# Optimization experiments

Measured on AMD Instinct MI355X. Metric: run time of the kernel, lower is better.

The kernel has to match this reference:

```python
import jax, jax.numpy as jnp
import numpy as np

B, S, D, H = 2, 2048, 1024, 16
DK = D // H

def setup_inputs() -> dict:
    key = jax.random.key(0)
    k1, k2, k3 = jax.random.split(key, 3)
    std = 2.0 / (D + 3 * D)
    x = jax.random.normal(k1, (B, S, D), dtype=jnp.float32)
    W_qkv = jax.random.normal(k2, (3 * D, D), dtype=jnp.float32) * std
    W_out = jax.random.normal(k3, (D, D), dtype=jnp.float32) * (2.0 / (2 * D))
    return {"x": x, "W_qkv": W_qkv, "W_out": W_out}

def reference(x, W_qkv, W_out):
    # fused QKV projection: [..., d_in] x [d_out, d_in] -> [..., d_out]
    proj = jnp.einsum('bsd,ed->bse', x, W_qkv)               # [B,S,3*H*DK]
    proj = proj.reshape(B, S, 3, H, DK)
    q = proj[:, :, 0].transpose(0, 2, 1, 3)                  # [B,H,S,DK]
    k = proj[:, :, 1].transpose(0, 2, 1, 3)
    v = proj[:, :, 2].transpose(0, 2, 1, 3)
    scores = jnp.einsum('bhnd,bhmd->bhnm', q, k) / jnp.sqrt(jnp.float32(DK))
    causal = jnp.tril(jnp.ones((S, S), dtype=bool))
    scores = jnp.where(causal, scores, -jnp.inf)
    attn = jax.nn.softmax(scores, axis=-1)
    out = jnp.einsum('bhnm,bhmd->bhnd', attn, v)             # [B,H,S,DK]
    out = out.transpose(0, 2, 1, 3).reshape(B, S, H * DK)
    return jnp.einsum('bsd,ed->bse', out, W_out)             # [B,S,D]
```

## Files before the change

kernel.cpp:

```cpp
#include <hip/hip_runtime.h>
#include <hip/hip_bf16.h>
#include <stdint.h>

typedef __attribute__((ext_vector_type(8))) __bf16 bf16x8;
typedef __attribute__((ext_vector_type(8))) short  short8;
typedef __attribute__((ext_vector_type(4))) float  f32x4;

#define MFMA16(a, b, c) __builtin_amdgcn_mfma_f32_16x16x32_bf16((a), (b), (c), 0, 0, 0)

__device__ __forceinline__ unsigned short f32_bf16(float f) {
  union { float f; unsigned u; } v; v.f = f;
  unsigned r = v.u + 0x7FFFu + ((v.u >> 16) & 1u);
  return (unsigned short)(r >> 16);
}

__device__ __forceinline__ void gload16(const unsigned short* g, unsigned short* l) {
  __builtin_amdgcn_global_load_lds(
      (const __attribute__((address_space(1))) unsigned int*)(g),
      (__attribute__((address_space(3))) unsigned int*)(l), 16, 0, 0);
}

__global__ void cvt3_kernel(const float* __restrict__ a, int na4,
                            const float* __restrict__ b, int nb4,
                            const float* __restrict__ c, int nc4,
                            unsigned short* __restrict__ oa,
                            unsigned short* __restrict__ ob,
                            unsigned short* __restrict__ oc) {
  int total = na4 + nb4 + nc4;
  for (int i = blockIdx.x * blockDim.x + threadIdx.x; i < total; i += gridDim.x * blockDim.x) {
    const float* src; unsigned short* dst; int j = i;
    if (j < na4) { src = a; dst = oa; }
    else if (j - na4 < nb4) { j -= na4; src = b; dst = ob; }
    else { j -= na4 + nb4; src = c; dst = oc; }
    float4 v = reinterpret_cast<const float4*>(src)[j];
    ushort4 o4;
    o4.x = f32_bf16(v.x); o4.y = f32_bf16(v.y);
    o4.z = f32_bf16(v.z); o4.w = f32_bf16(v.w);
    reinterpret_cast<ushort4*>(dst)[j] = o4;
  }
}

__global__ __launch_bounds__(512, 2) void gemm_qkv_8ph(const unsigned short* __restrict__ A,
                                                       const unsigned short* __restrict__ Bm,
                                                       unsigned short* __restrict__ qkv) {
  extern __shared__ unsigned short SM[];
  const int tid  = threadIdx.x;
  const int lane = tid & 63;
  const int w    = tid >> 6;
  const int wr   = w >> 2, wc = w & 3;
  const int l16  = lane & 15, lh = lane >> 4;
  const int sw   = l16 & 7;
  const int m0   = blockIdx.y * 256;
  const int n0   = blockIdx.x * 256;

  f32x4 acc[8][4];
#pragma unroll
  for (int mi = 0; mi < 8; ++mi)
#pragma unroll
    for (int ni = 0; ni < 4; ++ni) acc[mi][ni] = 0.f;

  const int r0 = tid >> 3,         h0 = (tid & 7) ^ (r0 & 7);
  const int r1 = (tid + 512) >> 3, h1 = (tid & 7) ^ (r1 & 7);
  const unsigned short* Asrc[2][2];
  const unsigned short* Bsrc[2][2];
  Asrc[0][0] = A + (size_t)(m0 + r0) * 1024 + h0 * 8;
  Asrc[0][1] = A + (size_t)(m0 + r1) * 1024 + h1 * 8;
  Asrc[1][0] = A + (size_t)(m0 + 128 + r0) * 1024 + h0 * 8;
  Asrc[1][1] = A + (size_t)(m0 + 128 + r1) * 1024 + h1 * 8;
  Bsrc[0][0] = Bm + (size_t)(n0 + r0) * 1024 + h0 * 8;
  Bsrc[0][1] = Bm + (size_t)(n0 + r1) * 1024 + h1 * 8;
  Bsrc[1][0] = Bm + (size_t)(n0 + 128 + r0) * 1024 + h0 * 8;
  Bsrc[1][1] = Bm + (size_t)(n0 + 128 + r1) * 1024 + h1 * 8;
  const int ld0 = (w * 64) * 8;
  const int ld1 = (512 + w * 64) * 8;

#define STAGE_A(buf, h, U) do { \
    gload16(Asrc[h][0] + (U) * 64, SM + (buf) * 32768 + (h) * 8192 + ld0); \
    gload16(Asrc[h][1] + (U) * 64, SM + (buf) * 32768 + (h) * 8192 + ld1); } while (0)
#define STAGE_B(buf, h, U) do { \
    gload16(Bsrc[h][0] + (U) * 64, SM + (buf) * 32768 + 16384 + (h) * 8192 + ld0); \
    gload16(Bsrc[h][1] + (U) * 64, SM + (buf) * 32768 + 16384 + (h) * 8192 + ld1); } while (0)

  STAGE_A(0, 0, 0); STAGE_A(0, 1, 0);
  STAGE_B(0, 0, 0); STAGE_B(0, 1, 0);
  STAGE_B(1, 0, 1); STAGE_B(1, 1, 1);
  asm volatile("s_waitcnt vmcnt(4)" ::: "memory");
  __builtin_amdgcn_s_barrier();

  const int NT = 16;
#pragma unroll 2
  for (int U = 0; U < NT; ++U) {
    const int b = U & 1;
    const unsigned short* Ab = SM + b * 32768 + wr * 8192;
    const unsigned short* Bb = SM + b * 32768 + 16384 + (wc >> 1) * 8192;
    const int rB = (wc & 1) * 64;
    bf16x8 bfr[4][2], af[2][2];

#define LDA(i, j) (*(const bf16x8*)(Ab + (((i) * 16 + l16) * 8 + (((j) * 4 + lh) ^ sw)) * 8))
#define LDB(n, j) (*(const bf16x8*)(Bb + (((rB + (n) * 16 + l16)) * 8 + (((j) * 4 + lh) ^ sw)) * 8))
#define PHASE_MFMA(p) \
    __builtin_amdgcn_s_setprio(1); \
    _Pragma("unroll") \
    for (int n = 0; n < 4; ++n) { \
      acc[2*(p)][n]   = MFMA16(af[0][0], bfr[n][0], acc[2*(p)][n]); \
      acc[2*(p)][n]   = MFMA16(af[0][1], bfr[n][1], acc[2*(p)][n]); \
      acc[2*(p)+1][n] = MFMA16(af[1][0], bfr[n][0], acc[2*(p)+1][n]); \
      acc[2*(p)+1][n] = MFMA16(af[1][1], bfr[n][1], acc[2*(p)+1][n]); \
    } \
    __builtin_amdgcn_s_setprio(0);

    af[0][0] = LDA(0, 0); af[0][1] = LDA(0, 1);
    af[1][0] = LDA(1, 0); af[1][1] = LDA(1, 1);
#pragma unroll
    for (int n = 0; n < 4; ++n) { bfr[n][0] = LDB(n, 0); bfr[n][1] = LDB(n, 1); }
    if (U + 1 < NT) STAGE_A(b ^ 1, 0, U + 1);
    __builtin_amdgcn_s_barrier();
    PHASE_MFMA(0)
    __builtin_amdgcn_s_barrier();
    af[0][0] = LDA(2, 0); af[0][1] = LDA(2, 1);
    af[1][0] = LDA(3, 0); af[1][1] = LDA(3, 1);
    if (U + 1 < NT) STAGE_A(b ^ 1, 1, U + 1);
    __builtin_amdgcn_s_barrier();
    PHASE_MFMA(1)
    __builtin_amdgcn_s_barrier();
    af[0][0] = LDA(4, 0); af[0][1] = LDA(4, 1);
    af[1][0] = LDA(5, 0); af[1][1] = LDA(5, 1);
    if (U + 2 < NT) STAGE_B(b, 0, U + 2);
    __builtin_amdgcn_s_barrier();
    PHASE_MFMA(2)
    __builtin_amdgcn_s_barrier();
    af[0][0] = LDA(6, 0); af[0][1] = LDA(6, 1);
    af[1][0] = LDA(7, 0); af[1][1] = LDA(7, 1);
    if (U + 2 < NT) STAGE_B(b, 1, U + 2);
    __builtin_amdgcn_s_barrier();
    PHASE_MFMA(3)
    asm volatile("s_waitcnt vmcnt(4)" ::: "memory");
    __builtin_amdgcn_s_barrier();
#undef LDA
#undef LDB
#undef PHASE_MFMA
  }

  __syncthreads();
  unsigned short* Ep = SM + w * 8192;
  const int gn0 = n0 + wc * 64;
  const int cc  = gn0 >> 10;
  const int hh2 = (gn0 & 1023) >> 6;
  const int gm0 = m0 + wr * 128;
  const int bb2 = gm0 >> 11;
  const int ss0 = gm0 & 2047;
  const int bh2 = bb2 * 16 + hh2;

  if (cc < 2) {
    const float qsc = (cc == 0) ? 0.18033688f : 1.0f;
#pragma unroll
    for (int mi = 0; mi < 8; ++mi)
#pragma unroll
      for (int ni = 0; ni < 4; ++ni)
#pragma unroll
        for (int r = 0; r < 4; ++r) {
          int row = mi * 16 + lh * 4 + r;
          int col = (ni * 16 + l16) ^ (lh << 3);
          Ep[row * 64 + col] = f32_bf16(acc[mi][ni][r] * qsc);
        }
    unsigned short* qk = qkv + (((size_t)cc * 32 + bh2) * 2048 + ss0) * 64;
#pragma unroll
    for (int it = 0; it < 16; ++it) {
      int ci = it * 64 + lane;
      int row = ci >> 3, c = ci & 7;
      short8 vv = *(const short8*)(Ep + row * 64 + ((c ^ ((row >> 2) & 3)) * 8));
      *(short8*)(qk + (size_t)row * 64 + c * 8) = vv;
    }
  } else {
#pragma unroll
    for (int mi = 0; mi < 8; ++mi)
#pragma unroll
      for (int ni = 0; ni < 4; ++ni) {
        int dk = ni * 16 + l16;
        int ssl = mi * 16 + lh * 4;
        unsigned lo, hi;
        asm("v_cvt_pk_bf16_f32 %0, %1, %2" : "=v"(lo) : "v"(acc[mi][ni][0]), "v"(acc[mi][ni][1]));
        asm("v_cvt_pk_bf16_f32 %0, %1, %2" : "=v"(hi) : "v"(acc[mi][ni][2]), "v"(acc[mi][ni][3]));
        int off = dk * 128 + (ssl ^ ((dk & 7) << 3));
        *(uint2*)(Ep + off) = make_uint2(lo, hi);
      }
    unsigned short* vt = qkv + (size_t)8388608 + (size_t)bh2 * 64 * 2048 + ss0;
#pragma unroll
    for (int it = 0; it < 16; ++it) {
      int ci = it * 64 + lane;
      int dk = ci >> 4, c = ci & 15;
      short8 vv = *(const short8*)(Ep + dk * 128 + ((c ^ (dk & 7)) * 8));
      *(short8*)(vt + (size_t)dk * 2048 + c * 8) = vv;
    }
  }
#undef STAGE_A
#undef STAGE_B
}

__global__ __launch_bounds__(256) void gemm_out(const unsigned short* __restrict__ A,
                                                const unsigned short* __restrict__ Bm,
                                                float* __restrict__ C,
                                                int M, int N, int K) {
  extern __shared__ unsigned short SM[];
  unsigned short* As = SM;
  unsigned short* Bs = SM + 4096;
  const int tid  = threadIdx.x;
  const int lane = tid & 63;
  const int wid  = tid >> 6;
  const int wr   = wid >> 1, wc = wid & 1;
  const int l16  = lane & 15, lh = lane >> 4;
  const int m0   = blockIdx.y * 128;
  const int n0   = blockIdx.x * 128;

  f32x4 acc[4][4];
#pragma unroll
  for (int mi = 0; mi < 4; ++mi)
#pragma unroll
    for (int ni = 0; ni < 4; ++ni) acc[mi][ni] = 0.f;

  const int c0 = tid, c1 = 256 + tid;
  const unsigned short* a0 = A + (size_t)(m0 + (c0 >> 2)) * K + (c0 & 3) * 8;
  const unsigned short* a1 = A + (size_t)(m0 + (c1 >> 2)) * K + (c1 & 3) * 8;
  const unsigned short* b0 = Bm + (size_t)(n0 + (c0 >> 2)) * K + (c0 & 3) * 8;
  const unsigned short* b1 = Bm + (size_t)(n0 + (c1 >> 2)) * K + (c1 & 3) * 8;
  const int d0 = wid * 64 * 8;
  const int d1 = (256 + wid * 64) * 8;

  for (int k0 = 0; k0 < K; k0 += 32) {
    __syncthreads();
    gload16(a0 + k0, As + d0);
    gload16(a1 + k0, As + d1);
    gload16(b0 + k0, Bs + d0);
    gload16(b1 + k0, Bs + d1);
    __syncthreads();
    bf16x8 af[4], bfr[4];
#pragma unroll
    for (int i = 0; i < 4; ++i) {
      af[i]  = *(const bf16x8*)(As + (wr * 64 + i * 16 + l16) * 32 + lh * 8);
      bfr[i] = *(const bf16x8*)(Bs + (wc * 64 + i * 16 + l16) * 32 + lh * 8);
    }
#pragma unroll
    for (int mi = 0; mi < 4; ++mi)
#pragma unroll
      for (int ni = 0; ni < 4; ++ni)
        acc[mi][ni] = MFMA16(af[mi], bfr[ni], acc[mi][ni]);
  }

  __syncthreads();
  float* Ef = (float*)(SM + wid * 4096);
  const int gm0 = m0 + wr * 64;
  const int gn0 = n0 + wc * 64;
#pragma unroll
  for (int p = 0; p < 2; ++p) {
#pragma unroll
    for (int mi = 0; mi < 4; ++mi)
#pragma unroll
      for (int q = 0; q < 2; ++q) {
        int ni = 2 * p + q;
#pragma unroll
        for (int r = 0; r < 4; ++r) {
          int row = mi * 16 + lh * 4 + r;
          int col = (q * 16 + l16) ^ ((row & 7) << 2);
          Ef[row * 32 + col] = acc[mi][ni][r];
        }
      }
#pragma unroll
    for (int it = 0; it < 8; ++it) {
      int ci = it * 64 + lane;
      int row = ci >> 3, c4 = ci & 7;
      float4 vv = *(const float4*)(Ef + row * 32 + ((c4 * 4) ^ ((row & 7) << 2)));
      *(float4*)(&C[(size_t)(gm0 + row) * N + gn0 + p * 32 + c4 * 4]) = vv;
    }
  }
}

__device__ const signed char JQT[48] = {31,31,30,15, 30,29,29,28,14, 28,27,27,26,13, 26,25,25,24,12,
                                        24,23,23,22,11, 22,21,21,20,10, 20,19,19,18, 9, 18,17,17,16, 8,
                                        16, 7, 6, 5, 4, 3, 2, 1, 0};
__device__ const signed char JS0[48] = { 0,16, 0, 0, 16, 0,15, 0, 0, 15, 0,14, 0, 0, 14, 0,13, 0, 0,
                                        13, 0,12, 0, 0, 12, 0,11, 0, 0, 11, 0,10, 0, 0, 10, 0, 9, 0, 0,
                                         9, 0, 0, 0, 0, 0, 0, 0, 0};
__device__ const signed char JNT[48] = {16,16,16,16, 15,15,15,15,15, 14,14,14,14,14, 13,13,13,13,13,
                                        12,12,12,12,12, 11,11,11,11,11, 10,10,10,10,10,  9, 9, 9, 9, 9,
                                         8, 8, 7, 6, 5, 4, 3, 2, 1};
__device__ const signed char JSL[48] = {30,31,28,-1, 29,26,27,24,-1, 25,22,23,20,-1, 21,18,19,16,-1,
                                        17,14,15,12,-1, 13,10,11, 8,-1,  9, 6, 7, 4,-1,  5, 2, 3, 0,-1,
                                         1,-1,-1,-1,-1,-1,-1,-1,-1};

__global__ __launch_bounds__(256) void attn_kernel(const unsigned short* __restrict__ Qg,
                                                   const unsigned short* __restrict__ Kg,
                                                   const unsigned short* __restrict__ Vtg,
                                                   unsigned short* __restrict__ Og,
                                                   char* __restrict__ parts) {
  __shared__ unsigned short Ks[2][64 * 64];
  __shared__ unsigned short Vs[2][64 * 64];
  __shared__ unsigned short Pl[4][16 * 64];

  const int tid  = threadIdx.x;
  const int lane = tid & 63;
  const int w    = tid >> 6;
  const int l16  = lane & 15, lh = lane >> 4;
  const int sw   = l16 & 7;

  const int jb   = blockIdx.x >> 5;
  const int bh   = blockIdx.x & 31;
  const int qt   = JQT[jb];
  const int ts0  = JS0[jb];
  const int tend = ts0 + JNT[jb];
  const int slot = JSL[jb];
  const int bb   = bh >> 4, hh = bh & 15;
  const int qb   = qt * 64;
  const int wqb  = qb + w * 16;

  const unsigned short* Qh = Qg + (size_t)bh * (2048 * 64);
  const unsigned short* Kh = Kg + (size_t)bh * (2048 * 64);
  const unsigned short* Vh = Vtg + (size_t)bh * (64 * 2048);

  bf16x8 qf[2];
#pragma unroll
  for (int h2 = 0; h2 < 2; ++h2)
    qf[h2] = *(const bf16x8*)(Qh + (size_t)(wqb + l16) * 64 + h2 * 32 + lh * 8);

  float mreg = 0.f;
  float ll   = 0.f;
  f32x4 o[4];
#pragma unroll
  for (int f = 0; f < 4; ++f) o[f] = 0.f;

  const int sA = tid, sB = tid + 256;
  const int rA = sA >> 3, hA = (sA & 7) ^ (rA & 7);
  const int rB = sB >> 3, hB = (sB & 7) ^ (rB & 7);
  const unsigned short* kSrcA = Kh + rA * 64 + hA * 8;
  const unsigned short* kSrcB = Kh + rB * 64 + hB * 8;
  const unsigned short* vSrcA = Vh + (size_t)rA * 2048 + hA * 8;
  const unsigned short* vSrcB = Vh + (size_t)rB * 2048 + hB * 8;
  const int ldsA = w * 64 * 8;
  const int ldsB = (256 + w * 64) * 8;

  gload16(kSrcA + (size_t)(ts0 * 64) * 64, &Ks[0][ldsA]);
  gload16(kSrcB + (size_t)(ts0 * 64) * 64, &Ks[0][ldsB]);
  gload16(vSrcA + ts0 * 64, &Vs[0][ldsA]);
  gload16(vSrcB + ts0 * 64, &Vs[0][ldsB]);
  __syncthreads();

  for (int t = ts0; t < tend; ++t) {
    const int kv0 = t * 64;
    const int cur = (t - ts0) & 1;
    if (t + 1 < tend) {
      const int nk = kv0 + 64;
      gload16(kSrcA + (size_t)nk * 64, &Ks[cur ^ 1][ldsA]);
      gload16(kSrcB + (size_t)nk * 64, &Ks[cur ^ 1][ldsB]);
      gload16(vSrcA + nk, &Vs[cur ^ 1][ldsA]);
      gload16(vSrcB + nk, &Vs[cur ^ 1][ldsB]);
    }

    {
      const unsigned short* Kb = Ks[cur];
      const unsigned short* Vb = Vs[cur];

      f32x4 st[4];
#pragma unroll
      for (int tt = 0; tt < 4; ++tt) {
        const unsigned short* krow = Kb + (tt * 16 + l16) * 64;
        bf16x8 kf0 = *(const bf16x8*)(krow + ((lh ^ sw) * 8));
        bf16x8 kf1 = *(const bf16x8*)(krow + (((lh + 4) ^ sw) * 8));
        f32x4 a = {0.f, 0.f, 0.f, 0.f};
        a = MFMA16(kf0, qf[0], a);
        a = MFMA16(kf1, qf[1], a);
        st[tt] = a;
      }

      if (kv0 + 63 > wqb) {
        int qrow = wqb + l16;
#pragma unroll
        for (int tt = 0; tt < 4; ++tt) {
          int kvb = kv0 + tt * 16 + lh * 4;
#pragma unroll
          for (int r = 0; r < 4; ++r)
            if (kvb + r > qrow) st[tt][r] = -__builtin_inff();
        }
      }

      float pm = fmaxf(fmaxf(st[0][0], st[0][1]), fmaxf(st[0][2], st[0][3]));
#pragma unroll
      for (int tt = 1; tt < 4; ++tt)
        pm = fmaxf(pm, fmaxf(fmaxf(st[tt][0], st[tt][1]), fmaxf(st[tt][2], st[tt][3])));
      if (!__all(pm <= mreg + 8.f)) {
        float t0 = pm;
        t0 = fmaxf(t0, __shfl_xor(t0, 16));
        t0 = fmaxf(t0, __shfl_xor(t0, 32));
        float mn = fmaxf(mreg, t0);
        float er = exp2f(mreg - mn);
        mreg = mn;
        ll *= er;
#pragma unroll
        for (int r = 0; r < 4; ++r) {
          float e = __shfl(er, lh * 4 + r);
#pragma unroll
          for (int f = 0; f < 4; ++f) o[f][r] *= e;
        }
      }

      unsigned short* Pw = Pl[w];
      int rbase = l16 * 64;
      float ps = 0.f;
#pragma unroll
      for (int tt = 0; tt < 4; ++tt) {
        float p0 = exp2f(st[tt][0] - mreg);
        float p1 = exp2f(st[tt][1] - mreg);
        float p2 = exp2f(st[tt][2] - mreg);
        float p3 = exp2f(st[tt][3] - mreg);
        ps += (p0 + p1) + (p2 + p3);
        unsigned lo, hi;
        asm("v_cvt_pk_bf16_f32 %0, %1, %2" : "=v"(lo) : "v"(p0), "v"(p1));
        asm("v_cvt_pk_bf16_f32 %0, %1, %2" : "=v"(hi) : "v"(p2), "v"(p3));
        int c8 = tt * 2 + (lh >> 1);
        int off = rbase + ((c8 ^ sw) << 3) + (lh & 1) * 4;
        *(uint2*)(Pw + off) = make_uint2(lo, hi);
      }
      float rs = ps;
      rs += __shfl_xor(rs, 16);
      rs += __shfl_xor(rs, 32);
      ll += rs;

      bf16x8 pf0 = *(const bf16x8*)(Pw + rbase + ((lh ^ sw) * 8));
      bf16x8 pf1 = *(const bf16x8*)(Pw + rbase + (((lh + 4) ^ sw) * 8));
#pragma unroll
      for (int f = 0; f < 4; ++f) {
        const unsigned short* vrow = Vb + (f * 16 + l16) * 64;
        bf16x8 vf0 = *(const bf16x8*)(vrow + ((lh ^ sw) * 8));
        bf16x8 vf1 = *(const bf16x8*)(vrow + (((lh + 4) ^ sw) * 8));
        o[f] = MFMA16(pf0, vf0, o[f]);
        o[f] = MFMA16(pf1, vf1, o[f]);
      }
    }
    __syncthreads();
  }

  if (slot < 0) {
    unsigned short* op = Og + (size_t)bb * 2048 * 1024 + (size_t)hh * 64;
#pragma unroll
    for (int r = 0; r < 4; ++r) {
      float linv = 1.f / __shfl(ll, lh * 4 + r);
      int row = wqb + lh * 4 + r;
#pragma unroll
      for (int f = 0; f < 4; ++f)
        op[(size_t)row * 1024 + f * 16 + l16] = f32_bf16(o[f][r] * linv);
    }
  } else {
    char* pb = parts + (size_t)(bh * 32 + slot) * 8704;
    float* pl = (float*)pb;
    float* pmv = pl + 64;
    unsigned short* pO = (unsigned short*)(pb + 512);
    float lv[4], mv[4];
#pragma unroll
    for (int r = 0; r < 4; ++r) {
      lv[r] = __shfl(ll, lh * 4 + r);
      mv[r] = __shfl(mreg, lh * 4 + r);
    }
    if (l16 == 0) {
#pragma unroll
      for (int r = 0; r < 4; ++r) {
        pl[w * 16 + lh * 4 + r]  = lv[r];
        pmv[w * 16 + lh * 4 + r] = mv[r];
      }
    }
#pragma unroll
    for (int r = 0; r < 4; ++r)
#pragma unroll
      for (int f = 0; f < 4; ++f)
        pO[(w * 16 + lh * 4 + r) * 64 + f * 16 + l16] = f32_bf16(o[f][r]);
  }
}

__global__ __launch_bounds__(256) void merge_kernel(const char* __restrict__ parts,
                                                    unsigned short* __restrict__ Og) {
  const int task = blockIdx.x;
  const int bh = task & 31, qi = task >> 5;
  const int qt = 16 + qi;
  const int bb = bh >> 4, hh = bh & 15;
  const int tid = threadIdx.x;
  const int r = tid >> 2, q = tid & 3;

  const char* pb1 = parts + (size_t)(bh * 32 + 2 * qi) * 8704;
  const char* pb2 = parts + (size_t)(bh * 32 + 2 * qi + 1) * 8704;
  const float* l1p = (const float*)pb1;
  const float* l2p = (const float*)pb2;
  float lv1 = l1p[r], mv1 = l1p[64 + r];
  float lv2 = l2p[r], mv2 = l2p[64 + r];
  float mx = fmaxf(mv1, mv2);
  float w1 = exp2f(mv1 - mx), w2 = exp2f(mv2 - mx);
  float inv = 1.f / (lv1 * w1 + lv2 * w2);
  float s1 = w1 * inv, s2 = w2 * inv;

  const unsigned short* O1 = (const unsigned short*)(pb1 + 512) + r * 64 + q * 16;
  const unsigned short* O2 = (const unsigned short*)(pb2 + 512) + r * 64 + q * 16;
  short8 a0 = *(const short8*)(O1);
  short8 a1 = *(const short8*)(O1 + 8);
  short8 b0 = *(const short8*)(O2);
  short8 b1 = *(const short8*)(O2 + 8);

  unsigned outw[8];
#pragma unroll
  for (int i = 0; i < 4; ++i) {
    float x0 = __builtin_bit_cast(float, ((unsigned)(unsigned short)a0[2 * i]) << 16) * s1 +
               __builtin_bit_cast(float, ((unsigned)(unsigned short)b0[2 * i]) << 16) * s2;
    float x1 = __builtin_bit_cast(float, ((unsigned)(unsigned short)a0[2 * i + 1]) << 16) * s1 +
               __builtin_bit_cast(float, ((unsigned)(unsigned short)b0[2 * i + 1]) << 16) * s2;
    asm("v_cvt_pk_bf16_f32 %0, %1, %2" : "=v"(outw[i]) : "v"(x0), "v"(x1));
    float y0 = __builtin_bit_cast(float, ((unsigned)(unsigned short)a1[2 * i]) << 16) * s1 +
               __builtin_bit_cast(float, ((unsigned)(unsigned short)b1[2 * i]) << 16) * s2;
    float y1 = __builtin_bit_cast(float, ((unsigned)(unsigned short)a1[2 * i + 1]) << 16) * s1 +
               __builtin_bit_cast(float, ((unsigned)(unsigned short)b1[2 * i + 1]) << 16) * s2;
    asm("v_cvt_pk_bf16_f32 %0, %1, %2" : "=v"(outw[4 + i]) : "v"(y0), "v"(y1));
  }
  unsigned short* op = Og + ((size_t)bb * 2048 + qt * 64 + r) * 1024 + hh * 64 + q * 16;
  *(uint4*)(op)     = make_uint4(outw[0], outw[1], outw[2], outw[3]);
  *(uint4*)(op + 8) = make_uint4(outw[4], outw[5], outw[6], outw[7]);
}

extern "C" void kernel_launch(void* const* d_in, const int* in_sizes, int n_in,
                              void* d_out, int out_size, void* d_ws, size_t ws_size,
                              hipStream_t stream) {
  const float* x    = (const float*)d_in[0];
  const float* Wqkv = (const float*)d_in[1];
  const float* Wout = (const float*)d_in[2];
  float* out = (float*)d_out;

  char* ws = (char*)d_ws;
  unsigned short* xb  = (unsigned short*)(ws);
  unsigned short* wqb = (unsigned short*)(ws + (size_t)8 * 1024 * 1024);
  unsigned short* wob = (unsigned short*)(ws + (size_t)14 * 1024 * 1024);
  unsigned short* qkv = (unsigned short*)(ws + (size_t)16 * 1024 * 1024);
  unsigned short* att = (unsigned short*)(ws + (size_t)40 * 1024 * 1024);
  char* parts = ws;

  static bool attr_set = false;
  if (!attr_set) {
    hipFuncSetAttribute((const void*)gemm_qkv_8ph,
                        hipFuncAttributeMaxDynamicSharedMemorySize, 131072);
    attr_set = true;
  }

  cvt3_kernel<<<2048, 256, 0, stream>>>(x, 4194304 / 4, Wqkv, 3145728 / 4,
                                        Wout, 1048576 / 4, xb, wqb, wob);

  gemm_qkv_8ph<<<dim3(12, 16), 512, 131072, stream>>>(xb, wqb, qkv);

  const unsigned short* Qp  = qkv;
  const unsigned short* Kp  = qkv + 4194304;
  const unsigned short* Vtp = qkv + 8388608;
  attn_kernel<<<1536, 256, 0, stream>>>(Qp, Kp, Vtp, att, parts);
  merge_kernel<<<512, 256, 0, stream>>>(parts, att);

  gemm_out<<<dim3(8, 32), 256, 32768, stream>>>(att, wob, out, 4096, 1024, 1024);
}
```

Before: 118.3 us.

## Rewrite attention inner loop with 32x32 MFMA and split-KV warps

After: 118.1 us. About the same (-0.1%).

```diff
diff --git a/kernel.cpp b/kernel.cpp
--- a/kernel.cpp
+++ b/kernel.cpp
@@ -2,11 +2,13 @@
 #include <hip/hip_bf16.h>
 #include <stdint.h>
 
-typedef __attribute__((ext_vector_type(8))) __bf16 bf16x8;
-typedef __attribute__((ext_vector_type(8))) short  short8;
-typedef __attribute__((ext_vector_type(4))) float  f32x4;
+typedef __attribute__((ext_vector_type(8)))  __bf16 bf16x8;
+typedef __attribute__((ext_vector_type(8)))  short  short8;
+typedef __attribute__((ext_vector_type(4)))  float  f32x4;
+typedef __attribute__((ext_vector_type(16))) float  f32x16;
 
 #define MFMA16(a, b, c) __builtin_amdgcn_mfma_f32_16x16x32_bf16((a), (b), (c), 0, 0, 0)
+#define MFMA32(a, b, c) __builtin_amdgcn_mfma_f32_32x32x16_bf16((a), (b), (c), 0, 0, 0)
 
 __device__ __forceinline__ unsigned short f32_bf16(float f) {
   union { float f; unsigned u; } v; v.f = f;
@@ -294,13 +296,13 @@
                                                    char* __restrict__ parts) {
   __shared__ unsigned short Ks[2][64 * 64];
   __shared__ unsigned short Vs[2][64 * 64];
-  __shared__ unsigned short Pl[4][16 * 64];
 
   const int tid  = threadIdx.x;
   const int lane = tid & 63;
   const int w    = tid >> 6;
-  const int l16  = lane & 15, lh = lane >> 4;
-  const int sw   = l16 & 7;
+  const int wq   = w & 1, wkv = w >> 1;
+  const int l31  = lane & 31, hi = lane >> 5;
+  const int rx0  = (l31 ^ (l31 >> 3)) & 7;
 
   const int jb   = blockIdx.x >> 5;
   const int bh   = blockIdx.x & 31;
@@ -310,31 +312,28 @@
   const int slot = JSL[jb];
   const int bb   = bh >> 4, hh = bh & 15;
   const int qb   = qt * 64;
-  const int wqb  = qb + w * 16;
+  const int qcol = qb + wq * 32 + l31;
 
   const unsigned short* Qh = Qg + (size_t)bh * (2048 * 64);
   const unsigned short* Kh = Kg + (size_t)bh * (2048 * 64);
   const unsigned short* Vh = Vtg + (size_t)bh * (64 * 2048);
 
-  bf16x8 qf[2];
-#pragma unroll
-  for (int h2 = 0; h2 < 2; ++h2)
-    qf[h2] = *(const bf16x8*)(Qh + (size_t)(wqb + l16) * 64 + h2 * 32 + lh * 8);
-
-  float mreg = 0.f;
-  float ll   = 0.f;
-  f32x4 o[4];
-#pragma unroll
-  for (int f = 0; f < 4; ++f) o[f] = 0.f;
+  bf16x8 qf[4];
+#pragma unroll
+  for (int ks = 0; ks < 4; ++ks)
+    qf[ks] = *(const bf16x8*)(Qh + (size_t)qcol * 64 + ks * 16 + hi * 8);
+
+  f32x16 o0 = 0.f, o1 = 0.f;
+  float mreg = 0.f, ll = 0.f;
 
   const int sA = tid, sB = tid + 256;
-  const int rA = sA >> 3, hA = (sA & 7) ^ (rA & 7);
-  const int rB = sB >> 3, hB = (sB & 7) ^ (rB & 7);
+  const int rA = sA >> 3, hA = (sA & 7) ^ ((rA ^ (rA >> 3)) & 7);
+  const int rB = sB >> 3, hB = (sB & 7) ^ ((rB ^ (rB >> 3)) & 7);
   const unsigned short* kSrcA = Kh + rA * 64 + hA * 8;
   const unsigned short* kSrcB = Kh + rB * 64 + hB * 8;
   const unsigned short* vSrcA = Vh + (size_t)rA * 2048 + hA * 8;
   const unsigned short* vSrcB = Vh + (size_t)rB * 2048 + hB * 8;
-  const int ldsA = w * 64 * 8;
+  const int ldsA = (w * 64) * 8;
   const int ldsB = (256 + w * 64) * 8;
 
   gload16(kSrcA + (size_t)(ts0 * 64) * 64, &Ks[0][ldsA]);
@@ -353,123 +352,135 @@
       gload16(vSrcA + nk, &Vs[cur ^ 1][ldsA]);
       gload16(vSrcB + nk, &Vs[cur ^ 1][ldsB]);
     }
-
-    {
-      const unsigned short* Kb = Ks[cur];
-      const unsigned short* Vb = Vs[cur];
-
-      f32x4 st[4];
-#pragma unroll
-      for (int tt = 0; tt < 4; ++tt) {
-        const unsigned short* krow = Kb + (tt * 16 + l16) * 64;
-        bf16x8 kf0 = *(const bf16x8*)(krow + ((lh ^ sw) * 8));
-        bf16x8 kf1 = *(const bf16x8*)(krow + (((lh + 4) ^ sw) * 8));
-        f32x4 a = {0.f, 0.f, 0.f, 0.f};
-        a = MFMA16(kf0, qf[0], a);
-        a = MFMA16(kf1, qf[1], a);
-        st[tt] = a;
+    const unsigned short* Kb = Ks[cur];
+    const unsigned short* Vb = Vs[cur];
+
+    f32x16 s = 0.f;
+    const int kvl = wkv * 32 + l31;
+#pragma unroll
+    for (int ks = 0; ks < 4; ++ks) {
+      int c = (ks * 2 + hi) ^ rx0 ^ (wkv << 2);
+      bf16x8 ka = *(const bf16x8*)(Kb + kvl * 64 + c * 8);
+      s = MFMA32(ka, qf[ks], s);
+    }
+
+    if (t == qt) {
+#pragma unroll
+      for (int r = 0; r < 16; ++r) {
+        int kvp = kv0 + wkv * 32 + (r & 3) + 8 * (r >> 2) + 4 * hi;
+        if (kvp > qcol) s[r] = -__builtin_inff();
       }
-
-      if (kv0 + 63 > wqb) {
-        int qrow = wqb + l16;
-#pragma unroll
-        for (int tt = 0; tt < 4; ++tt) {
-          int kvb = kv0 + tt * 16 + lh * 4;
-#pragma unroll
-          for (int r = 0; r < 4; ++r)
-            if (kvb + r > qrow) st[tt][r] = -__builtin_inff();
-        }
+    }
+
+    float pm = s[0];
+#pragma unroll
+    for (int r = 1; r < 16; ++r) pm = fmaxf(pm, s[r]);
+    if (!__all(pm <= mreg + 8.f)) {
+      float t0 = fmaxf(pm, __shfl_xor(pm, 32));
+      float mn = fmaxf(mreg, t0);
+      float esc = exp2f(mreg - mn);
+      mreg = mn; ll *= esc;
+#pragma unroll
+      for (int r = 0; r < 16; ++r) { o0[r] *= esc; o1[r] *= esc; }
+    }
+
+    float p[16];
+#pragma unroll
+    for (int r = 0; r < 16; ++r) p[r] = exp2f(s[r] - mreg);
+    float ps = p[0];
+#pragma unroll
+    for (int r = 1; r < 16; ++r) ps += p[r];
+    ps += __shfl_xor(ps, 32);
+    ll += ps;
+
+    bf16x8 pf[2];
+#pragma unroll
+    for (int ks = 0; ks < 2; ++ks) {
+      const int off = ks * 8;
+      unsigned a1, b1, a2, b2;
+      asm("v_cvt_pk_bf16_f32 %0, %1, %2" : "=v"(a1) : "v"(p[off + 0]), "v"(p[off + 1]));
+      asm("v_cvt_pk_bf16_f32 %0, %1, %2" : "=v"(b1) : "v"(p[off + 4]), "v"(p[off + 5]));
+      asm("v_cvt_pk_bf16_f32 %0, %1, %2" : "=v"(a2) : "v"(p[off + 2]), "v"(p[off + 3]));
+      asm("v_cvt_pk_bf16_f32 %0, %1, %2" : "=v"(b2) : "v"(p[off + 6]), "v"(p[off + 7]));
+      asm("v_permlane32_swap_b32 %0, %1" : "+v"(a1), "+v"(b1));
+      asm("v_permlane32_swap_b32 %0, %1" : "+v"(a2), "+v"(b2));
+      union { unsigned u[4]; bf16x8 f; } fr;
+      fr.u[0] = a1; fr.u[1] = a2; fr.u[2] = b1; fr.u[3] = b2;
+      pf[ks] = fr.f;
+    }
+
+#pragma unroll
+    for (int ks = 0; ks < 2; ++ks) {
+      int cbase = wkv * 4 + ks * 2 + hi;
+      bf16x8 va0 = *(const bf16x8*)(Vb + l31 * 64 + (cbase ^ rx0) * 8);
+      bf16x8 va1 = *(const bf16x8*)(Vb + (32 + l31) * 64 + (cbase ^ rx0 ^ 4) * 8);
+      o0 = MFMA32(va0, pf[ks], o0);
+      o1 = MFMA32(va1, pf[ks], o1);
+    }
+    __syncthreads();
+  }
+
+  float* oxch = (float*)Ks;
+  float* lmx  = (float*)Vs;
+  if (wkv == 1) {
+    float* dst = oxch + wq * 2048;
+#pragma unroll
+    for (int r = 0; r < 16; ++r) {
+      int d0 = (r & 3) + 8 * (r >> 2) + 4 * hi;
+      dst[d0 * 32 + l31] = o0[r];
+      dst[(32 + d0) * 32 + l31] = o1[r];
+    }
+    if (hi == 0) { lmx[wq * 64 + l31] = ll; lmx[wq * 64 + 32 + l31] = mreg; }
+  }
+  __syncthreads();
+  if (wkv == 0) {
+    float lB = lmx[wq * 64 + l31];
+    float mB = lmx[wq * 64 + 32 + l31];
+    float mx = fmaxf(mreg, mB);
+    float wA = exp2f(mreg - mx), wB = exp2f(mB - mx);
+    float lT = ll * wA + lB * wB;
+    float inv = (slot < 0) ? (1.f / lT) : 1.f;
+    float sA2 = wA * inv, sB2 = wB * inv;
+    const float* src = oxch + wq * 2048;
+    unsigned short* slab = (unsigned short*)((char*)Vs + 1024) + wq * 2048;
+#pragma unroll
+    for (int i = 0; i < 8; ++i) {
+      int r = 2 * i;
+      int d0 = (r & 3) + 8 * (r >> 2) + 4 * hi;
+      float x0 = o0[r] * sA2 + src[d0 * 32 + l31] * sB2;
+      float x1 = o0[r + 1] * sA2 + src[(d0 + 1) * 32 + l31] * sB2;
+      float y0 = o1[r] * sA2 + src[(32 + d0) * 32 + l31] * sB2;
+      float y1 = o1[r + 1] * sA2 + src[(33 + d0) * 32 + l31] * sB2;
+      unsigned u0, u1;
+      asm("v_cvt_pk_bf16_f32 %0, %1, %2" : "=v"(u0) : "v"(x0), "v"(x1));
+      asm("v_cvt_pk_bf16_f32 %0, %1, %2" : "=v"(u1) : "v"(y0), "v"(y1));
+      *(unsigned*)(slab + l31 * 64 + (((d0 >> 3) ^ (l31 & 7)) * 8) + (d0 & 7)) = u0;
+      int d1 = 32 + d0;
+      *(unsigned*)(slab + l31 * 64 + (((d1 >> 3) ^ (l31 & 7)) * 8) + (d1 & 7)) = u1;
+    }
+    if (slot < 0) {
+      unsigned short* op = Og + (size_t)bb * 2048 * 1024 + (size_t)hh * 64;
+#pragma unroll
+      for (int it = 0; it < 4; ++it) {
+        int ci = it * 64 + lane;
+        int qr = ci >> 3, c = ci & 7;
+        short8 vv = *(const short8*)(slab + qr * 64 + ((c ^ (qr & 7)) * 8));
+        *(short8*)(op + (size_t)(qb + wq * 32 + qr) * 1024 + c * 8) = vv;
       }
-
-      float pm = fmaxf(fmaxf(st[0][0], st[0][1]), fmaxf(st[0][2], st[0][3]));
-#pragma unroll
-      for (int tt = 1; tt < 4; ++tt)
-        pm = fmaxf(pm, fmaxf(fmaxf(st[tt][0], st[tt][1]), fmaxf(st[tt][2], st[tt][3])));
-      if (!__all(pm <= mreg + 8.f)) {
-        float t0 = pm;
-        t0 = fmaxf(t0, __shfl_xor(t0, 16));
-        t0 = fmaxf(t0, __shfl_xor(t0, 32));
-        float mn = fmaxf(mreg, t0);
-        float er = exp2f(mreg - mn);
-        mreg = mn;
-        ll *= er;
-#pragma unroll
-        for (int r = 0; r < 4; ++r) {
-          float e = __shfl(er, lh * 4 + r);
-#pragma unroll
-          for (int f = 0; f < 4; ++f) o[f][r] *= e;
-        }
+    } else {
+      char* pb = parts + (size_t)(bh * 32 + slot) * 8704;
+      float* pl = (float*)pb;
+      float* pmv = pl + 64;
+      unsigned short* pO = (unsigned short*)(pb + 512);
+      if (hi == 0) { pl[wq * 32 + l31] = lT; pmv[wq * 32 + l31] = mx; }
+#pragma unroll
+      for (int it = 0; it < 4; ++it) {
+        int ci = it * 64 + lane;
+        int qr = ci >> 3, c = ci & 7;
+        short8 vv = *(const short8*)(slab + qr * 64 + ((c ^ (qr & 7)) * 8));
+        *(short8*)(pO + (size_t)(wq * 32 + qr) * 64 + c * 8) = vv;
       }
-
-      unsigned short* Pw = Pl[w];
-      int rbase = l16 * 64;
-      float ps = 0.f;
-#pragma unroll
-      for (int tt = 0; tt < 4; ++tt) {
-        float p0 = exp2f(st[tt][0] - mreg);
-        float p1 = exp2f(st[tt][1] - mreg);
-        float p2 = exp2f(st[tt][2] - mreg);
-        float p3 = exp2f(st[tt][3] - mreg);
-        ps += (p0 + p1) + (p2 + p3);
-        unsigned lo, hi;
-        asm("v_cvt_pk_bf16_f32 %0, %1, %2" : "=v"(lo) : "v"(p0), "v"(p1));
-        asm("v_cvt_pk_bf16_f32 %0, %1, %2" : "=v"(hi) : "v"(p2), "v"(p3));
-        int c8 = tt * 2 + (lh >> 1);
-        int off = rbase + ((c8 ^ sw) << 3) + (lh & 1) * 4;
-        *(uint2*)(Pw + off) = make_uint2(lo, hi);
-      }
-      float rs = ps;
-      rs += __shfl_xor(rs, 16);
-      rs += __shfl_xor(rs, 32);
-      ll += rs;
-
-      bf16x8 pf0 = *(const bf16x8*)(Pw + rbase + ((lh ^ sw) * 8));
-      bf16x8 pf1 = *(const bf16x8*)(Pw + rbase + (((lh + 4) ^ sw) * 8));
-#pragma unroll
-      for (int f = 0; f < 4; ++f) {
-        const unsigned short* vrow = Vb + (f * 16 + l16) * 64;
-        bf16x8 vf0 = *(const bf16x8*)(vrow + ((lh ^ sw) * 8));
-        bf16x8 vf1 = *(const bf16x8*)(vrow + (((lh + 4) ^ sw) * 8));
-        o[f] = MFMA16(pf0, vf0, o[f]);
-        o[f] = MFMA16(pf1, vf1, o[f]);
-      }
-    }
-    __syncthreads();
-  }
-
-  if (slot < 0) {
-    unsigned short* op = Og + (size_t)bb * 2048 * 1024 + (size_t)hh * 64;
-#pragma unroll
-    for (int r = 0; r < 4; ++r) {
-      float linv = 1.f / __shfl(ll, lh * 4 + r);
-      int row = wqb + lh * 4 + r;
-#pragma unroll
-      for (int f = 0; f < 4; ++f)
-        op[(size_t)row * 1024 + f * 16 + l16] = f32_bf16(o[f][r] * linv);
-    }
-  } else {
-    char* pb = parts + (size_t)(bh * 32 + slot) * 8704;
-    float* pl = (float*)pb;
-    float* pmv = pl + 64;
-    unsigned short* pO = (unsigned short*)(pb + 512);
-    float lv[4], mv[4];
-#pragma unroll
-    for (int r = 0; r < 4; ++r) {
-      lv[r] = __shfl(ll, lh * 4 + r);
-      mv[r] = __shfl(mreg, lh * 4 + r);
-    }
-    if (l16 == 0) {
-#pragma unroll
-      for (int r = 0; r < 4; ++r) {
-        pl[w * 16 + lh * 4 + r]  = lv[r];
-        pmv[w * 16 + lh * 4 + r] = mv[r];
-      }
-    }
-#pragma unroll
-    for (int r = 0; r < 4; ++r)
-#pragma unroll
-      for (int f = 0; f < 4; ++f)
-        pO[(w * 16 + lh * 4 + r) * 64 + f * 16 + l16] = f32_bf16(o[f][r]);
+    }
   }
 }
 
```
